# Performance work log

Measured on AMD Instinct MI355X. Metric: run time of the kernel, lower is better.

The kernel has to match this reference:

```python
import jax, jax.numpy as jnp
import numpy as np

MIN_SEGMENT_PIXELS = 50
NUM_SEG_IDS = 32  # segment ids in [0, 32); 0 = background


def setup_inputs() -> dict:
    key = jax.random.key(0)
    k1, k2 = jax.random.split(key)
    B, H, W = 16, 512, 1024
    flow = jax.random.normal(k1, (B, 2, H, W), dtype=jnp.float32)
    masks = jax.random.randint(k2, (B, H, W), 0, NUM_SEG_IDS, dtype=jnp.int32)
    return {"flow": flow, "masks": masks}


def reference(flow, masks):
    B, _, H, W = flow.shape
    S = NUM_SEG_IDS
    # Global segment id = b * S + seg_id so one fused segment_sum covers all batches.
    gid = (masks.reshape(B, -1) + jnp.arange(B, dtype=masks.dtype)[:, None] * S).reshape(-1)
    u = flow[:, 0].reshape(-1)
    v = flow[:, 1].reshape(-1)
    nseg = B * S
    cnt = jax.ops.segment_sum(jnp.ones_like(u), gid, num_segments=nseg)
    su  = jax.ops.segment_sum(u,     gid, num_segments=nseg)
    suu = jax.ops.segment_sum(u * u, gid, num_segments=nseg)
    sv  = jax.ops.segment_sum(v,     gid, num_segments=nseg)
    svv = jax.ops.segment_sum(v * v, gid, num_segments=nseg)
    safe_cnt = jnp.maximum(cnt, 1.0)
    denom = jnp.maximum(cnt - 1.0, 1.0)  # torch .var() is unbiased (ddof=1)
    var_u = (suu - su * su / safe_cnt) / denom
    var_v = (svv - sv * sv / safe_cnt) / denom
    is_bg = (jnp.arange(nseg) % S) == 0  # seg_id == 0 skipped
    valid = (cnt >= MIN_SEGMENT_PIXELS) & (~is_bg)
    total = jnp.sum(jnp.where(valid, var_u + var_v, 0.0))
    n = jnp.sum(valid.astype(flow.dtype))
    return jnp.where(n > 0, total / jnp.maximum(n, 1.0), 0.0)
```

## Files before the change

### kernel.cpp

```cpp
#include <hip/hip_runtime.h>

#define BATCH 16
#define NSEG 32
#define HW (512 * 1024)
#define MIN_PIX 50.0f

#define THREADS 64
#define CHUNKS 64
#define PIX_PER_BLOCK (HW / CHUNKS)
#define VEC 4
#define ITERS (PIX_PER_BLOCK / (THREADS * VEC))

#define ACC_FLOATS (BATCH * NSEG * 4)

__global__ __launch_bounds__(THREADS) void ovl_accum(
    const float* __restrict__ flow,
    const int* __restrict__ masks,
    float* __restrict__ acc)
{
    __shared__ float4 bins[THREADS][NSEG];

    const int tid = threadIdx.x;
    #pragma unroll
    for (int i = 0; i < NSEG; ++i)
        bins[tid][i] = make_float4(0.0f, 0.0f, 0.0f, 0.0f);
    __syncthreads();

    const int b = blockIdx.y;
    const int chunk = blockIdx.x;
    const float* __restrict__ u_base = flow + (size_t)b * 2 * HW;
    const float* __restrict__ v_base = u_base + HW;
    const int*   __restrict__ m_base = masks + (size_t)b * HW;
    const int p0 = chunk * PIX_PER_BLOCK;

#define LOADP(S, IT) { const int p = p0 + ((IT) * THREADS + tid) * VEC;        \
        m##S = *(const int4*)(m_base + p);                                    \
        u##S = *(const float4*)(u_base + p);                                  \
        v##S = *(const float4*)(v_base + p); }

#define PROC1(mm, uu, vv) { const int s = (mm) & (NSEG - 1);                   \
        float4 cur = bins[tid][s];                                            \
        cur.x += 1.0f; cur.y += (uu); cur.z += (vv);                          \
        cur.w += (uu) * (uu) + (vv) * (vv);                                   \
        bins[tid][s] = cur; }

#define PROCP(S) { PROC1(m##S.x, u##S.x, v##S.x) PROC1(m##S.y, u##S.y, v##S.y) \
        PROC1(m##S.z, u##S.z, v##S.z) PROC1(m##S.w, u##S.w, v##S.w) }

    int4 mA, mB; float4 uA, vA, uB, vB;
    LOADP(A, 0)
    LOADP(B, 1)
    #pragma unroll
    for (int it = 0; it < ITERS; it += 2) {
        PROCP(A)
        if (it + 2 < ITERS) LOADP(A, it + 2)
        PROCP(B)
        if (it + 3 < ITERS) LOADP(B, it + 3)
    }
    __syncthreads();

    const float* smf = (const float*)bins;
    #pragma unroll
    for (int pair = tid; pair < NSEG * 4; pair += THREADS) {
        float sum = 0.0f;
        #pragma unroll
        for (int j = 0; j < THREADS; ++j)
            sum += smf[j * NSEG * 4 + pair];
        unsafeAtomicAdd(&acc[(size_t)b * NSEG * 4 + pair], sum);
    }
}

__global__ __launch_bounds__(BATCH * NSEG) void ovl_finalize(
    const float* __restrict__ acc,
    float* __restrict__ out)
{
    const int tid = threadIdx.x;
    const float cnt = acc[tid * 4 + 0];
    const float su  = acc[tid * 4 + 1];
    const float sv  = acc[tid * 4 + 2];
    const float s2  = acc[tid * 4 + 3];

    const bool is_bg = (tid & (NSEG - 1)) == 0;
    const bool valid = (cnt >= MIN_PIX) && !is_bg;

    const float safe_cnt = fmaxf(cnt, 1.0f);
    const float denom = fmaxf(cnt - 1.0f, 1.0f);
    const float var_sum = (s2 - (su * su + sv * sv) / safe_cnt) / denom;

    float t = valid ? var_sum : 0.0f;
    float n = valid ? 1.0f : 0.0f;

    #pragma unroll
    for (int off = 32; off >= 1; off >>= 1) {
        t += __shfl_down(t, off, 64);
        n += __shfl_down(n, off, 64);
    }

    __shared__ float st[8], sn[8];
    const int wave = tid >> 6;
    const int lane = tid & 63;
    if (lane == 0) { st[wave] = t; sn[wave] = n; }
    __syncthreads();

    if (tid == 0) {
        float tot = 0.0f, ntot = 0.0f;
        #pragma unroll
        for (int w = 0; w < 8; ++w) { tot += st[w]; ntot += sn[w]; }
        out[0] = (ntot > 0.0f) ? (tot / fmaxf(ntot, 1.0f)) : 0.0f;
    }
}

extern "C" void kernel_launch(void* const* d_in, const int* in_sizes, int n_in,
                              void* d_out, int out_size, void* d_ws, size_t ws_size,
                              hipStream_t stream) {
    const float* flow = (const float*)d_in[0];
    const int* masks  = (const int*)d_in[1];
    float* out = (float*)d_out;
    float* acc = (float*)d_ws;

    hipMemsetAsync(acc, 0, ACC_FLOATS * sizeof(float), stream);

    dim3 grid(CHUNKS, BATCH);
    ovl_accum<<<grid, THREADS, 0, stream>>>(flow, masks, acc);
    ovl_finalize<<<1, BATCH * NSEG, 0, stream>>>(acc, out);
}
```

Before: 31.10 us.

## Replace memset and atomics with per-block partials and deeper interleaved loads

Each accumulation block now writes its 128 per-segment sums to its own slot in a partials buffer, and a 1024-thread finalize kernel reduces those slots before computing variances. This removes the workspace memset launch and the global atomic adds. The pixel mapping also changes so consecutive blocks read adjacent 1 KB strips of each image instead of contiguous chunks, and the software prefetch is four loads deep instead of two. In exchange, the finalize kernel must read all 1024x128 partial values, and each thread keeps more load registers live.

Result: slower. 34.23 us (+10.1%).

```diff
diff --git a/kernel.cpp b/kernel.cpp
--- a/kernel.cpp
+++ b/kernel.cpp
@@ -7,16 +7,14 @@
 
 #define THREADS 64
 #define CHUNKS 64
-#define PIX_PER_BLOCK (HW / CHUNKS)
-#define VEC 4
-#define ITERS (PIX_PER_BLOCK / (THREADS * VEC))
+#define QUADS 32
 
-#define ACC_FLOATS (BATCH * NSEG * 4)
+#define PART_STRIDE 128
 
 __global__ __launch_bounds__(THREADS) void ovl_accum(
     const float* __restrict__ flow,
     const int* __restrict__ masks,
-    float* __restrict__ acc)
+    float* __restrict__ partials)
 {
     __shared__ float4 bins[THREADS][NSEG];
 
@@ -24,71 +22,97 @@
     #pragma unroll
     for (int i = 0; i < NSEG; ++i)
         bins[tid][i] = make_float4(0.0f, 0.0f, 0.0f, 0.0f);
-    __syncthreads();
 
-    const int b = blockIdx.y;
-    const int chunk = blockIdx.x;
+    const int bid = blockIdx.x;
+    const int b  = bid >> 6;
+    const int bk = bid & (CHUNKS - 1);
     const float* __restrict__ u_base = flow + (size_t)b * 2 * HW;
     const float* __restrict__ v_base = u_base + HW;
     const int*   __restrict__ m_base = masks + (size_t)b * HW;
-    const int p0 = chunk * PIX_PER_BLOCK;
 
-#define LOADP(S, IT) { const int p = p0 + ((IT) * THREADS + tid) * VEC;        \
-        m##S = *(const int4*)(m_base + p);                                    \
-        u##S = *(const float4*)(u_base + p);                                  \
+#define LOADP(S, Q) { const int p = (((Q) * CHUNKS + bk) * THREADS + tid) * 4; \
+        m##S = *(const int4*)(m_base + p);                                     \
+        u##S = *(const float4*)(u_base + p);                                   \
         v##S = *(const float4*)(v_base + p); }
 
-#define PROC1(mm, uu, vv) { const int s = (mm) & (NSEG - 1);                   \
-        float4 cur = bins[tid][s];                                            \
-        cur.x += 1.0f; cur.y += (uu); cur.z += (vv);                          \
-        cur.w += (uu) * (uu) + (vv) * (vv);                                   \
-        bins[tid][s] = cur; }
+#define PX(mm, uu, vv) {                                                    \
+        const int   s  = (mm) & (NSEG - 1);                                 \
+        const float u_ = (uu), v_ = (vv);                                   \
+        float4 cur = bins[tid][s];                                          \
+        cur.x += 1.0f;                                                      \
+        cur.y += u_;                                                        \
+        cur.z += v_;                                                        \
+        cur.w += fmaf(u_, u_, v_ * v_);                                     \
+        bins[tid][s] = cur;                                                 \
+    }
 
-#define PROCP(S) { PROC1(m##S.x, u##S.x, v##S.x) PROC1(m##S.y, u##S.y, v##S.y) \
-        PROC1(m##S.z, u##S.z, v##S.z) PROC1(m##S.w, u##S.w, v##S.w) }
+#define PROCQ(mq, uq, vq) { PX(mq.x, uq.x, vq.x) PX(mq.y, uq.y, vq.y)       \
+                            PX(mq.z, uq.z, vq.z) PX(mq.w, uq.w, vq.w) }
 
-    int4 mA, mB; float4 uA, vA, uB, vB;
+    int4 mA, mB, mC, mD; float4 uA, vA, uB, vB, uC, vC, uD, vD;
     LOADP(A, 0)
     LOADP(B, 1)
+    LOADP(C, 2)
+    LOADP(D, 3)
     #pragma unroll
-    for (int it = 0; it < ITERS; it += 2) {
-        PROCP(A)
-        if (it + 2 < ITERS) LOADP(A, it + 2)
-        PROCP(B)
-        if (it + 3 < ITERS) LOADP(B, it + 3)
+    for (int q = 0; q < QUADS; q += 4) {
+        PROCQ(mA, uA, vA)
+        if (q + 4 < QUADS) LOADP(A, q + 4)
+        PROCQ(mB, uB, vB)
+        if (q + 5 < QUADS) LOADP(B, q + 5)
+        PROCQ(mC, uC, vC)
+        if (q + 6 < QUADS) LOADP(C, q + 6)
+        PROCQ(mD, uD, vD)
+        if (q + 7 < QUADS) LOADP(D, q + 7)
+    }
+
+    __syncthreads();
+
+    const float* bf = (const float*)bins;
+    #pragma unroll
+    for (int h = 0; h < 2; ++h) {
+        const int pair = tid + h * 64;
+        float sum = 0.0f;
+        #pragma unroll
+        for (int j = 0; j < THREADS; ++j)
+            sum += bf[j * (NSEG * 4) + pair];
+        partials[(size_t)bid * PART_STRIDE + pair] = sum;
+    }
+}
+
+__global__ __launch_bounds__(1024) void ovl_finalize(
+    const float* __restrict__ partials,
+    float* __restrict__ out)
+{
+    __shared__ float sums[BATCH * NSEG * 4];
+    const int tid = threadIdx.x;
+
+    #pragma unroll
+    for (int h = 0; h < 2; ++h) {
+        const int T = tid + h * 1024;
+        const int b = T >> 7, sc = T & 127;
+        float sum = 0.0f;
+        #pragma unroll 8
+        for (int j = 0; j < CHUNKS; ++j)
+            sum += partials[(size_t)(b * CHUNKS + j) * PART_STRIDE + sc];
+        sums[T] = sum;
     }
     __syncthreads();
 
-    const float* smf = (const float*)bins;
-    #pragma unroll
-    for (int pair = tid; pair < NSEG * 4; pair += THREADS) {
-        float sum = 0.0f;
-        #pragma unroll
-        for (int j = 0; j < THREADS; ++j)
-            sum += smf[j * NSEG * 4 + pair];
-        unsafeAtomicAdd(&acc[(size_t)b * NSEG * 4 + pair], sum);
+    float t = 0.0f, n = 0.0f;
+    if (tid < BATCH * NSEG) {
+        const float cnt = sums[tid * 4 + 0];
+        const float su  = sums[tid * 4 + 1];
+        const float sv  = sums[tid * 4 + 2];
+        const float s2  = sums[tid * 4 + 3];
+        const bool is_bg = (tid & (NSEG - 1)) == 0;
+        const bool valid = (cnt >= MIN_PIX) && !is_bg;
+        const float safe_cnt = fmaxf(cnt, 1.0f);
+        const float denom = fmaxf(cnt - 1.0f, 1.0f);
+        const float var_sum = (s2 - (su * su + sv * sv) / safe_cnt) / denom;
+        t = valid ? var_sum : 0.0f;
+        n = valid ? 1.0f : 0.0f;
     }
-}
-
-__global__ __launch_bounds__(BATCH * NSEG) void ovl_finalize(
-    const float* __restrict__ acc,
-    float* __restrict__ out)
-{
-    const int tid = threadIdx.x;
-    const float cnt = acc[tid * 4 + 0];
-    const float su  = acc[tid * 4 + 1];
-    const float sv  = acc[tid * 4 + 2];
-    const float s2  = acc[tid * 4 + 3];
-
-    const bool is_bg = (tid & (NSEG - 1)) == 0;
-    const bool valid = (cnt >= MIN_PIX) && !is_bg;
-
-    const float safe_cnt = fmaxf(cnt, 1.0f);
-    const float denom = fmaxf(cnt - 1.0f, 1.0f);
-    const float var_sum = (s2 - (su * su + sv * sv) / safe_cnt) / denom;
-
-    float t = valid ? var_sum : 0.0f;
-    float n = valid ? 1.0f : 0.0f;
 
     #pragma unroll
     for (int off = 32; off >= 1; off >>= 1) {
@@ -96,7 +120,7 @@
         n += __shfl_down(n, off, 64);
     }
 
-    __shared__ float st[8], sn[8];
+    __shared__ float st[16], sn[16];
     const int wave = tid >> 6;
     const int lane = tid & 63;
     if (lane == 0) { st[wave] = t; sn[wave] = n; }
@@ -116,11 +140,8 @@
     const float* flow = (const float*)d_in[0];
     const int* masks  = (const int*)d_in[1];
     float* out = (float*)d_out;
-    float* acc = (float*)d_ws;
+    float* partials = (float*)d_ws;
 
-    hipMemsetAsync(acc, 0, ACC_FLOATS * sizeof(float), stream);
-
-    dim3 grid(CHUNKS, BATCH);
-    ovl_accum<<<grid, THREADS, 0, stream>>>(flow, masks, acc);
-    ovl_finalize<<<1, BATCH * NSEG, 0, stream>>>(acc, out);
+    ovl_accum<<<BATCH * CHUNKS, THREADS, 0, stream>>>(flow, masks, partials);
+    ovl_finalize<<<1, 1024, 0, stream>>>(partials, out);
 }
```
